# Kernel optimization log

Hardware: AMD Instinct MI355X
Metric: run time of the kernel (lower is better)

Reference implementation:

```python
import jax, jax.numpy as jnp
import numpy as np

B, S, D, H = 2, 2048, 1024, 16
HD = D // H
EPS = 1e-5

def gelu_tanh(x):
    # GPT-2 tanh approximation of GELU
    c = np.sqrt(2.0 / np.pi).astype(np.float32)
    return 0.5 * x * (1.0 + jnp.tanh(c * (x + 0.044715 * x * x * x)))

def layernorm(x, gamma, beta):
    mu = jnp.mean(x, axis=-1, keepdims=True)
    var = jnp.mean(jnp.square(x - mu), axis=-1, keepdims=True)
    return (x - mu) * jax.lax.rsqrt(var + EPS) * gamma + beta

def setup_inputs() -> dict:
    key = jax.random.key(0)
    ks = jax.random.split(key, 16)
    std = 0.02
    def w(k, shape):
        return jax.random.normal(k, shape, dtype=jnp.float32) * std
    return {
        "x": jax.random.normal(ks[0], (B, S, D), dtype=jnp.float32),
        "Wq": w(ks[1], (D, D)), "bq": jnp.zeros((D,), jnp.float32),
        "Wk": w(ks[2], (D, D)), "bk": jnp.zeros((D,), jnp.float32),
        "Wv": w(ks[3], (D, D)), "bv": jnp.zeros((D,), jnp.float32),
        "Wp": w(ks[4], (D, D)), "bp": jnp.zeros((D,), jnp.float32),
        "g0": jnp.ones((D,), jnp.float32), "beta0": jnp.zeros((D,), jnp.float32),
        "W1": w(ks[5], (D, 4 * D)), "b1": jnp.zeros((4 * D,), jnp.float32),
        "W2": w(ks[6], (4 * D, D)), "b2": jnp.zeros((D,), jnp.float32),
        "g1": jnp.ones((D,), jnp.float32), "beta1": jnp.zeros((D,), jnp.float32),
    }

def reference(x, Wq, bq, Wk, bk, Wv, bv, Wp, bp, g0, beta0, W1, b1, W2, b2, g1, beta1):
    b, s, d = x.shape
    # --- causal self-attention (naive full score matrix, as in source) ---
    q = (x @ Wq + bq).reshape(b, s, H, HD).transpose(0, 2, 1, 3)  # [b,h,s,hd]
    k = (x @ Wk + bk).reshape(b, s, H, HD).transpose(0, 2, 1, 3)
    v = (x @ Wv + bv).reshape(b, s, H, HD).transpose(0, 2, 1, 3)
    scores = jnp.einsum('bhqd,bhkd->bhqk', q, k) * (1.0 / np.sqrt(HD))
    mask = jnp.tril(jnp.ones((s, s), dtype=x.dtype))  # lower-triangular causal mask
    scores = scores * mask - 1e10 * (1.0 - mask)
    attn = jax.nn.softmax(scores, axis=-1)
    y = jnp.einsum('bhqk,bhkd->bhqd', attn, v)
    y = y.transpose(0, 2, 1, 3).reshape(b, s, d)
    a = y @ Wp + bp
    # --- post-LN MLP block ---
    x = x + a
    h = layernorm(x, g0, beta0)
    h = gelu_tanh(h @ W1 + b1)
    h = h @ W2 + b2
    x = x + h
    return layernorm(x, g1, beta1)
```

## Files before the change

### kernel.cpp

```cpp
#include <hip/hip_runtime.h>
#include <stdint.h>

#define S_LEN 2048
#define DIM   1024
#define NH    16
#define HDIM  64
#define MTOK  4096
#define DFF   4096

#define QS 0.18033688011112042f

typedef short bf16x8 __attribute__((ext_vector_type(8)));
typedef float f32x4  __attribute__((ext_vector_type(4)));
typedef float f32x16 __attribute__((ext_vector_type(16)));
typedef unsigned int u32x4 __attribute__((ext_vector_type(4)));

__device__ __forceinline__ unsigned short f2bf(float f) {
  unsigned int u = __float_as_uint(f);
  u += 0x7fffu + ((u >> 16) & 1u);
  return (unsigned short)(u >> 16);
}

__device__ __forceinline__ unsigned cvtpk(float a, float b) {
  unsigned r;
  asm("v_cvt_pk_bf16_f32 %0, %1, %2" : "=v"(r) : "v"(a), "v"(b));
  return r;
}

__device__ __forceinline__ float gelu_f(float x) {
  const float c = 0.7978845608028654f;
  float u = c * (x + 0.044715f * x * x * x);
  return 0.5f * x * (1.0f + tanhf(u));
}

__device__ __forceinline__ void gld_lds16(const void* g, void* lds) {
  using gu32p = __attribute__((address_space(1))) unsigned int*;
  using lu32p = __attribute__((address_space(3))) unsigned int*;
  __builtin_amdgcn_global_load_lds((gu32p)g, (lu32p)lds, 16, 0, 0);
}

__global__ __launch_bounds__(256) void cast_f32_bf16(const float* __restrict__ x,
                                                     unsigned short* __restrict__ xb) {
  const size_t i = (size_t)blockIdx.x * 256 + threadIdx.x;
  const float4 a = ((const float4*)x)[2 * i];
  const float4 b = ((const float4*)x)[2 * i + 1];
  ushort4 p0, p1;
  p0.x = f2bf(a.x); p0.y = f2bf(a.y); p0.z = f2bf(a.z); p0.w = f2bf(a.w);
  p1.x = f2bf(b.x); p1.y = f2bf(b.y); p1.z = f2bf(b.z); p1.w = f2bf(b.w);
  ((ushort4*)xb)[2 * i]     = p0;
  ((ushort4*)xb)[2 * i + 1] = p1;
}

__global__ __launch_bounds__(256) void tcast_k(const float* __restrict__ W,
                                               unsigned short* __restrict__ Wt,
                                               int K, int N, float scale) {
  __shared__ float tile[32][33];
  const int tx = threadIdx.x & 31, ty = threadIdx.x >> 5;
  const int n0 = blockIdx.x * 32, k0 = blockIdx.y * 32;
#pragma unroll
  for (int i = 0; i < 4; i++)
    tile[ty + 8 * i][tx] = W[(size_t)(k0 + ty + 8 * i) * N + n0 + tx];
  __syncthreads();
#pragma unroll
  for (int i = 0; i < 4; i++)
    Wt[(size_t)(n0 + ty + 8 * i) * K + k0 + tx] = f2bf(tile[tx][ty + 8 * i] * scale);
}

__global__ __launch_bounds__(256) void bcat_k(const float* __restrict__ bq,
                                              const float* __restrict__ bk,
                                              const float* __restrict__ bv,
                                              float* __restrict__ bqkv) {
  const int t = blockIdx.x * 256 + threadIdx.x;
  float v;
  if (t < 1024)      v = bq[t] * QS;
  else if (t < 2048) v = bk[t - 1024];
  else               v = bv[t - 2048];
  bqkv[t] = v;
}

__global__ __launch_bounds__(256) void vtrans_k(const unsigned short* __restrict__ qkv,
                                                unsigned short* __restrict__ vT) {
  __shared__ unsigned short tile[64][65];
  const int bh = blockIdx.y, b = bh >> 4, h = bh & 15;
  const int s0 = blockIdx.x * 64;
  const int t = threadIdx.x;
#pragma unroll
  for (int i = 0; i < 16; i++) {
    int idx = i * 256 + t, r = idx >> 6, c = idx & 63;
    tile[r][c] = qkv[(size_t)(b * S_LEN + s0 + r) * 3072 + 2048 + h * HDIM + c];
  }
  __syncthreads();
#pragma unroll
  for (int i = 0; i < 16; i++) {
    int idx = i * 256 + t, d = idx >> 6, s = idx & 63;
    vT[(size_t)(bh * HDIM + d) * S_LEN + s0 + s] = tile[s][d];
  }
}

template <int EPI>
__global__ __launch_bounds__(256) void gemm_bt(const unsigned short* __restrict__ A,
                                               const unsigned short* __restrict__ Bt,
                                               const float* __restrict__ bias,
                                               const float* __restrict__ resid,
                                               void* __restrict__ Cout,
                                               int M, int N, int K) {
  __shared__ alignas(16) short As[128 * 32];
  __shared__ alignas(16) short Bs[128 * 32];
  const int t = threadIdx.x;
  const int w = t >> 6, lane = t & 63;
  const int m0 = blockIdx.y * 128, n0 = blockIdx.x * 128;
  const int wr = (w >> 1) * 64, wc = (w & 1) * 64;
  const int lr = lane & 15, lg = lane >> 4;

  f32x4 acc[4][4] = {};

  const int off0 = w * 2048 + lane * 16;
  const int r0 = off0 >> 6, c0 = (off0 & 63) >> 1;
  const int off1 = off0 + 1024;
  const int r1 = off1 >> 6, c1 = (off1 & 63) >> 1;

  const unsigned short* Ag0 = A + (size_t)(m0 + r0) * K + c0;
  const unsigned short* Ag1 = A + (size_t)(m0 + r1) * K + c1;
  const unsigned short* Bg0 = Bt + (size_t)(n0 + r0) * K + c0;
  const unsigned short* Bg1 = Bt + (size_t)(n0 + r1) * K + c1;
  char* AsB = (char*)As;
  char* BsB = (char*)Bs;

  for (int k0 = 0; k0 < K; k0 += 32) {
    gld_lds16(Ag0 + k0, AsB + w * 2048);
    gld_lds16(Ag1 + k0, AsB + w * 2048 + 1024);
    gld_lds16(Bg0 + k0, BsB + w * 2048);
    gld_lds16(Bg1 + k0, BsB + w * 2048 + 1024);
    __syncthreads();
    bf16x8 af[4], bfr[4];
#pragma unroll
    for (int i = 0; i < 4; i++) {
      af[i]  = *reinterpret_cast<const bf16x8*>(As + (wr + i * 16 + lr) * 32 + lg * 8);
      bfr[i] = *reinterpret_cast<const bf16x8*>(Bs + (wc + i * 16 + lr) * 32 + lg * 8);
    }
#pragma unroll
    for (int mi = 0; mi < 4; mi++)
#pragma unroll
      for (int ni = 0; ni < 4; ni++)
        acc[mi][ni] = __builtin_amdgcn_mfma_f32_16x16x32_bf16(af[mi], bfr[ni],
                                                              acc[mi][ni], 0, 0, 0);
    __syncthreads();
  }

  const int colb = n0 + wc + lr;
  const int rowb = m0 + wr + lg * 4;
#pragma unroll
  for (int ni = 0; ni < 4; ni++) {
    const int col = colb + ni * 16;
    const float bv = bias[col];
#pragma unroll
    for (int mi = 0; mi < 4; mi++) {
#pragma unroll
      for (int j = 0; j < 4; j++) {
        const int row = rowb + mi * 16 + j;
        const size_t idx = (size_t)row * N + col;
        float v = acc[mi][ni][j] + bv;
        if constexpr (EPI == 0) {
          ((unsigned short*)Cout)[idx] = f2bf(v);
        } else if constexpr (EPI == 1) {
          ((unsigned short*)Cout)[idx] = f2bf(gelu_f(v));
        } else {
          ((float*)Cout)[idx] = v + resid[idx];
        }
      }
    }
  }
}

__global__ __launch_bounds__(128) void attn32_k(const unsigned short* __restrict__ qkv,
                                                const unsigned short* __restrict__ vT,
                                                unsigned short* __restrict__ y) {
  __shared__ float smem[2][64][33];
  __shared__ float msh[2][64], lsh[2][64];

  const int t = threadIdx.x, w = t >> 6, lane = t & 63;
  const int ql = lane & 31, hi = lane >> 5;
  const int bh = blockIdx.x, bb = bh >> 4, hh = bh & 15;
  const int qt = 63 - blockIdx.y;
  const int half = w;
  const int q0 = qt * 32;

  const unsigned short* qp = qkv + (size_t)(bb * S_LEN + q0 + ql) * 3072 + hh * HDIM + hi * 8;
  const bf16x8 qf0 = *(const bf16x8*)(qp);
  const bf16x8 qf1 = *(const bf16x8*)(qp + 16);
  const bf16x8 qf2 = *(const bf16x8*)(qp + 32);
  const bf16x8 qf3 = *(const bf16x8*)(qp + 48);

  const unsigned short* kbp = qkv + (size_t)(bb * S_LEN) * 3072 + 1024 + hh * HDIM + hi * 8;
  const unsigned short* vbp = vT + (size_t)(bh * HDIM + ql) * (size_t)S_LEN + hi * 8;

  f32x16 acc0 = {}, acc1 = {};
  float m = -1e30f, l = 0.f;

  const int start = half * 32;

  const unsigned short* kp0 = kbp + (size_t)(start + ql) * 3072;
  bf16x8 kc0 = *(const bf16x8*)(kp0);
  bf16x8 kc1 = *(const bf16x8*)(kp0 + 16);
  bf16x8 kc2 = *(const bf16x8*)(kp0 + 32);
  bf16x8 kc3 = *(const bf16x8*)(kp0 + 48);

  for (int t0 = start; t0 <= q0; t0 += 64) {
    const unsigned short* vp = vbp + t0;
    const bf16x8 vf0 = *(const bf16x8*)(vp);
    const bf16x8 vf1 = *(const bf16x8*)(vp + 32 * S_LEN);
    const bf16x8 vf2 = *(const bf16x8*)(vp + 16);
    const bf16x8 vf3 = *(const bf16x8*)(vp + 32 * S_LEN + 16);

    __builtin_amdgcn_s_setprio(1);
    f32x16 st = {};
    st = __builtin_amdgcn_mfma_f32_32x32x16_bf16(kc0, qf0, st, 0, 0, 0);
    st = __builtin_amdgcn_mfma_f32_32x32x16_bf16(kc1, qf1, st, 0, 0, 0);
    st = __builtin_amdgcn_mfma_f32_32x32x16_bf16(kc2, qf2, st, 0, 0, 0);
    st = __builtin_amdgcn_mfma_f32_32x32x16_bf16(kc3, qf3, st, 0, 0, 0);
    __builtin_amdgcn_s_setprio(0);

    const int t1 = (t0 + 64 <= q0) ? (t0 + 64) : t0;
    const unsigned short* kpn = kbp + (size_t)(t1 + ql) * 3072;
    const bf16x8 kn0 = *(const bf16x8*)(kpn);
    const bf16x8 kn1 = *(const bf16x8*)(kpn + 16);
    const bf16x8 kn2 = *(const bf16x8*)(kpn + 32);
    const bf16x8 kn3 = *(const bf16x8*)(kpn + 48);

    if (t0 == q0) {
#pragma unroll
      for (int r = 0; r < 16; r++) {
        const int key = (r & 3) + 8 * (r >> 2) + 4 * hi;
        if (key > ql) st[r] = -1e30f;
      }
    }
    float pm = st[0];
#pragma unroll
    for (int r = 1; r < 16; r++) pm = fmaxf(pm, st[r]);
    pm = fmaxf(pm, __shfl_xor(pm, 32));
    if (!__all(pm - m <= 8.f)) {
      const float mn = fmaxf(m, pm);
      const float rs = exp2f(m - mn);
      l *= rs;
#pragma unroll
      for (int r = 0; r < 16; r++) { acc0[r] *= rs; acc1[r] *= rs; }
      m = mn;
    }
    float sum = 0.f;
#pragma unroll
    for (int r = 0; r < 16; r++) { st[r] = exp2f(st[r] - m); sum += st[r]; }
    sum += __shfl_xor(sum, 32);
    l += sum;

    {
      const unsigned c0 = cvtpk(st[0], st[1]), c1 = cvtpk(st[2], st[3]);
      const unsigned c2 = cvtpk(st[4], st[5]), c3 = cvtpk(st[6], st[7]);
      const unsigned x0 = __shfl_xor(c0, 32), x1 = __shfl_xor(c1, 32);
      const unsigned x2 = __shfl_xor(c2, 32), x3 = __shfl_xor(c3, 32);
      u32x4 fu;
      fu.x = hi ? x2 : c0; fu.y = hi ? x3 : c1;
      fu.z = hi ? c2 : x0; fu.w = hi ? c3 : x1;
      const bf16x8 pf = __builtin_bit_cast(bf16x8, fu);
      __builtin_amdgcn_s_setprio(1);
      acc0 = __builtin_amdgcn_mfma_f32_32x32x16_bf16(vf0, pf, acc0, 0, 0, 0);
      acc1 = __builtin_amdgcn_mfma_f32_32x32x16_bf16(vf1, pf, acc1, 0, 0, 0);
      __builtin_amdgcn_s_setprio(0);
    }
    {
      const unsigned c4 = cvtpk(st[8], st[9]),   c5 = cvtpk(st[10], st[11]);
      const unsigned c6 = cvtpk(st[12], st[13]), c7 = cvtpk(st[14], st[15]);
      const unsigned x4 = __shfl_xor(c4, 32), x5 = __shfl_xor(c5, 32);
      const unsigned x6 = __shfl_xor(c6, 32), x7 = __shfl_xor(c7, 32);
      u32x4 fu;
      fu.x = hi ? x6 : c4; fu.y = hi ? x7 : c5;
      fu.z = hi ? c6 : x4; fu.w = hi ? c7 : x5;
      const bf16x8 pf = __builtin_bit_cast(bf16x8, fu);
      __builtin_amdgcn_s_setprio(1);
      acc0 = __builtin_amdgcn_mfma_f32_32x32x16_bf16(vf2, pf, acc0, 0, 0, 0);
      acc1 = __builtin_amdgcn_mfma_f32_32x32x16_bf16(vf3, pf, acc1, 0, 0, 0);
      __builtin_amdgcn_s_setprio(0);
    }
    kc0 = kn0; kc1 = kn1; kc2 = kn2; kc3 = kn3;
  }

#pragma unroll
  for (int r = 0; r < 16; r++) {
    smem[w][lane][r]      = acc0[r];
    smem[w][lane][16 + r] = acc1[r];
  }
  msh[w][lane] = m; lsh[w][lane] = l;
  __syncthreads();
  if (half) return;

  const int pw = w ^ 1;
  const float mB = msh[pw][lane], lB = lsh[pw][lane];
  const float mm = fmaxf(m, mB);
  float sA = exp2f(m - mm), sB = exp2f(mB - mm);
  const float linv = 1.f / (l * sA + lB * sB);
  sA *= linv; sB *= linv;

  unsigned* tp = (unsigned*)&smem[w][0][0];
  const float* pa = &smem[pw][lane][0];
#pragma unroll
  for (int j = 0; j < 8; j++) {
    const int wd = (j & 1) + 4 * (j >> 1) + 2 * hi;
    const float a0 = acc0[2 * j] * sA + pa[2 * j] * sB;
    const float b0 = acc0[2 * j + 1] * sA + pa[2 * j + 1] * sB;
    tp[ql * 34 + wd] = cvtpk(a0, b0);
    const float a1 = acc1[2 * j] * sA + pa[16 + 2 * j] * sB;
    const float b1 = acc1[2 * j + 1] * sA + pa[16 + 2 * j + 1] * sB;
    tp[ql * 34 + 16 + wd] = cvtpk(a1, b1);
  }
  unsigned* yu = (unsigned*)y;
  const size_t yrow = (size_t)(bb * S_LEN + q0 + ql) * (DIM / 2) + hh * (HDIM / 2) + hi * 16;
#pragma unroll
  for (int i = 0; i < 8; i++) {
    const uint2 d2 = *(const uint2*)&tp[ql * 34 + hi * 16 + 2 * i];
    *(uint2*)&yu[yrow + 2 * i] = d2;
  }
}

template <int OUTBF>
__global__ __launch_bounds__(256) void ln_k(const float* __restrict__ X,
                                            const float* __restrict__ g,
                                            const float* __restrict__ be,
                                            void* __restrict__ out) {
  const int row = blockIdx.x, t = threadIdx.x;
  const float4 v = ((const float4*)(X + (size_t)row * DIM))[t];
  float s  = v.x + v.y + v.z + v.w;
  float s2 = v.x * v.x + v.y * v.y + v.z * v.z + v.w * v.w;
#pragma unroll
  for (int o = 32; o >= 1; o >>= 1) {
    s  += __shfl_down(s, o);
    s2 += __shfl_down(s2, o);
  }
  __shared__ float red[8];
  if ((t & 63) == 0) { red[t >> 6] = s; red[4 + (t >> 6)] = s2; }
  __syncthreads();
  s  = red[0] + red[1] + red[2] + red[3];
  s2 = red[4] + red[5] + red[6] + red[7];
  const float mu  = s * (1.0f / DIM);
  const float var = s2 * (1.0f / DIM) - mu * mu;
  const float r   = rsqrtf(var + 1e-5f);
  const float4 gv = ((const float4*)g)[t];
  const float4 bv = ((const float4*)be)[t];
  const float o0 = (v.x - mu) * r * gv.x + bv.x;
  const float o1 = (v.y - mu) * r * gv.y + bv.y;
  const float o2 = (v.z - mu) * r * gv.z + bv.z;
  const float o3 = (v.w - mu) * r * gv.w + bv.w;
  if constexpr (OUTBF) {
    ushort4 p; p.x = f2bf(o0); p.y = f2bf(o1); p.z = f2bf(o2); p.w = f2bf(o3);
    ((ushort4*)out)[(size_t)row * 256 + t] = p;
  } else {
    float4 p; p.x = o0; p.y = o1; p.z = o2; p.w = o3;
    ((float4*)out)[(size_t)row * 256 + t] = p;
  }
}

extern "C" void kernel_launch(void* const* d_in, const int* in_sizes, int n_in,
                              void* d_out, int out_size, void* d_ws, size_t ws_size,
                              hipStream_t stream) {
  const float* x   = (const float*)d_in[0];
  const float* Wq  = (const float*)d_in[1];
  const float* bq  = (const float*)d_in[2];
  const float* Wk  = (const float*)d_in[3];
  const float* bk  = (const float*)d_in[4];
  const float* Wv  = (const float*)d_in[5];
  const float* bv  = (const float*)d_in[6];
  const float* Wp  = (const float*)d_in[7];
  const float* bp  = (const float*)d_in[8];
  const float* g0  = (const float*)d_in[9];
  const float* be0 = (const float*)d_in[10];
  const float* W1  = (const float*)d_in[11];
  const float* b1  = (const float*)d_in[12];
  const float* W2  = (const float*)d_in[13];
  const float* b2  = (const float*)d_in[14];
  const float* g1  = (const float*)d_in[15];
  const float* be1 = (const float*)d_in[16];

  char* ws = (char*)d_ws;
  const size_t MB = 1ull << 20;
  unsigned short* xb    = (unsigned short*)(ws + 0 * MB);
  unsigned short* qkvb  = (unsigned short*)(ws + 8 * MB);
  unsigned short* vTb   = (unsigned short*)(ws + 32 * MB);
  unsigned short* yb    = (unsigned short*)(ws + 40 * MB);
  float*          bqkv  = (float*)(ws + 48 * MB);
  float*          x1    = (float*)(ws + 48 * MB);
  unsigned short* hb    = (unsigned short*)(ws + 64 * MB);
  unsigned short* WqkvT = (unsigned short*)(ws + 72 * MB);
  unsigned short* WpT   = (unsigned short*)(ws + 78 * MB);
  unsigned short* W1T   = (unsigned short*)(ws + 80 * MB);
  unsigned short* W2T   = (unsigned short*)(ws + 88 * MB);
  unsigned short* h1    = (unsigned short*)(ws + 8 * MB);
  float*          x2    = (float*)(ws + 64 * MB);

  cast_f32_bf16<<<2048, 256, 0, stream>>>(x, xb);
  tcast_k<<<dim3(32, 32), 256, 0, stream>>>(Wq, WqkvT,               1024, 1024, QS);
  tcast_k<<<dim3(32, 32), 256, 0, stream>>>(Wk, WqkvT + 1024 * 1024, 1024, 1024, 1.f);
  tcast_k<<<dim3(32, 32), 256, 0, stream>>>(Wv, WqkvT + 2048 * 1024, 1024, 1024, 1.f);
  tcast_k<<<dim3(32, 32), 256, 0, stream>>>(Wp, WpT, 1024, 1024, 1.f);
  tcast_k<<<dim3(128, 32), 256, 0, stream>>>(W1, W1T, 1024, 4096, 1.f);
  tcast_k<<<dim3(32, 128), 256, 0, stream>>>(W2, W2T, 4096, 1024, 1.f);
  bcat_k<<<12, 256, 0, stream>>>(bq, bk, bv, bqkv);

  gemm_bt<0><<<dim3(24, 32), 256, 0, stream>>>(xb, WqkvT, bqkv, nullptr, qkvb, MTOK, 3072, 1024);

  vtrans_k<<<dim3(32, 32), 256, 0, stream>>>(qkvb, vTb);
  attn32_k<<<dim3(32, 64), 128, 0, stream>>>(qkvb, vTb, yb);

  gemm_bt<2><<<dim3(8, 32), 256, 0, stream>>>(yb, WpT, bp, x, x1, MTOK, DIM, DIM);
  ln_k<1><<<4096, 256, 0, stream>>>(x1, g0, be0, hb);

  gemm_bt<1><<<dim3(32, 32), 256, 0, stream>>>(hb, W1T, b1, nullptr, h1, MTOK, DFF, DIM);
  gemm_bt<2><<<dim3(8, 32), 256, 0, stream>>>(h1, W2T, b2, x1, x2, MTOK, DIM, DFF);
  ln_k<0><<<4096, 256, 0, stream>>>(x2, g1, be1, d_out);
}
```

Measured before the change: 471.8 us.

## Double-buffer GEMM LDS tiles with K=64 steps and block swizzle

```diff
diff --git a/kernel.cpp b/kernel.cpp
--- a/kernel.cpp
+++ b/kernel.cpp
@@ -98,53 +98,71 @@
 }
 
 template <int EPI>
-__global__ __launch_bounds__(256) void gemm_bt(const unsigned short* __restrict__ A,
-                                               const unsigned short* __restrict__ Bt,
-                                               const float* __restrict__ bias,
-                                               const float* __restrict__ resid,
-                                               void* __restrict__ Cout,
-                                               int M, int N, int K) {
-  __shared__ alignas(16) short As[128 * 32];
-  __shared__ alignas(16) short Bs[128 * 32];
-  const int t = threadIdx.x;
-  const int w = t >> 6, lane = t & 63;
-  const int m0 = blockIdx.y * 128, n0 = blockIdx.x * 128;
+__global__ __launch_bounds__(256, 2) void gemm2p(const unsigned short* __restrict__ A,
+                                                 const unsigned short* __restrict__ Bt,
+                                                 const float* __restrict__ bias,
+                                                 const float* __restrict__ resid,
+                                                 void* __restrict__ Cout,
+                                                 int M, int N, int K) {
+  __shared__ alignas(16) short As[2][128 * 64];
+  __shared__ alignas(16) short Bs[2][128 * 64];
+  const int t = threadIdx.x, w = t >> 6, lane = t & 63;
+
+  const int gx = gridDim.x, nwg = gx * gridDim.y;
+  const int bid = blockIdx.x + gx * blockIdx.y;
+  const int swz = (bid & 7) * (nwg >> 3) + (bid >> 3);
+  const int m0 = (swz / gx) * 128, n0 = (swz % gx) * 128;
+
   const int wr = (w >> 1) * 64, wc = (w & 1) * 64;
   const int lr = lane & 15, lg = lane >> 4;
 
   f32x4 acc[4][4] = {};
 
-  const int off0 = w * 2048 + lane * 16;
-  const int r0 = off0 >> 6, c0 = (off0 & 63) >> 1;
-  const int off1 = off0 + 1024;
-  const int r1 = off1 >> 6, c1 = (off1 & 63) >> 1;
-
-  const unsigned short* Ag0 = A + (size_t)(m0 + r0) * K + c0;
-  const unsigned short* Ag1 = A + (size_t)(m0 + r1) * K + c1;
-  const unsigned short* Bg0 = Bt + (size_t)(n0 + r0) * K + c0;
-  const unsigned short* Bg1 = Bt + (size_t)(n0 + r1) * K + c1;
-  char* AsB = (char*)As;
-  char* BsB = (char*)Bs;
-
-  for (int k0 = 0; k0 < K; k0 += 32) {
-    gld_lds16(Ag0 + k0, AsB + w * 2048);
-    gld_lds16(Ag1 + k0, AsB + w * 2048 + 1024);
-    gld_lds16(Bg0 + k0, BsB + w * 2048);
-    gld_lds16(Bg1 + k0, BsB + w * 2048 + 1024);
+  const int sr = w * 32 + (lane >> 3);
+  const int sc = (lane & 7) * 8;
+  const unsigned short* Ag = A + (size_t)(m0 + sr) * K + sc;
+  const unsigned short* Bg = Bt + (size_t)(n0 + sr) * K + sc;
+  const int dbase = w * 4096 + lane * 16;
+
+  const int NT = K >> 6;
+
+#pragma unroll
+  for (int i = 0; i < 4; i++) {
+    gld_lds16(Ag + (size_t)(i * 8) * K, (char*)As[0] + dbase + i * 1024);
+    gld_lds16(Bg + (size_t)(i * 8) * K, (char*)Bs[0] + dbase + i * 1024);
+  }
+  __syncthreads();
+
+  int cur = 0;
+  for (int kt = 0; kt < NT; ++kt) {
+    if (kt + 1 < NT) {
+      const int k1 = (kt + 1) << 6;
+#pragma unroll
+      for (int i = 0; i < 4; i++) {
+        gld_lds16(Ag + (size_t)(i * 8) * K + k1, (char*)As[cur ^ 1] + dbase + i * 1024);
+        gld_lds16(Bg + (size_t)(i * 8) * K + k1, (char*)Bs[cur ^ 1] + dbase + i * 1024);
+      }
+    }
+    bf16x8 af[2][4], bfr[2][4];
+#pragma unroll
+    for (int ks = 0; ks < 2; ks++)
+#pragma unroll
+      for (int i = 0; i < 4; i++) {
+        af[ks][i]  = *reinterpret_cast<const bf16x8*>(&As[cur][(wr + i * 16 + lr) * 64 + ks * 32 + lg * 8]);
+        bfr[ks][i] = *reinterpret_cast<const bf16x8*>(&Bs[cur][(wc + i * 16 + lr) * 64 + ks * 32 + lg * 8]);
+      }
+    __builtin_amdgcn_s_setprio(1);
+#pragma unroll
+    for (int ks = 0; ks < 2; ks++)
+#pragma unroll
+      for (int mi = 0; mi < 4; mi++)
+#pragma unroll
+        for (int ni = 0; ni < 4; ni++)
+          acc[mi][ni] = __builtin_amdgcn_mfma_f32_16x16x32_bf16(af[ks][mi], bfr[ks][ni],
+                                                                acc[mi][ni], 0, 0, 0);
+    __builtin_amdgcn_s_setprio(0);
     __syncthreads();
-    bf16x8 af[4], bfr[4];
-#pragma unroll
-    for (int i = 0; i < 4; i++) {
-      af[i]  = *reinterpret_cast<const bf16x8*>(As + (wr + i * 16 + lr) * 32 + lg * 8);
-      bfr[i] = *reinterpret_cast<const bf16x8*>(Bs + (wc + i * 16 + lr) * 32 + lg * 8);
-    }
-#pragma unroll
-    for (int mi = 0; mi < 4; mi++)
-#pragma unroll
-      for (int ni = 0; ni < 4; ni++)
-        acc[mi][ni] = __builtin_amdgcn_mfma_f32_16x16x32_bf16(af[mi], bfr[ni],
-                                                              acc[mi][ni], 0, 0, 0);
-    __syncthreads();
+    cur ^= 1;
   }
 
   const int colb = n0 + wc + lr;
@@ -403,15 +421,15 @@
   tcast_k<<<dim3(32, 128), 256, 0, stream>>>(W2, W2T, 4096, 1024, 1.f);
   bcat_k<<<12, 256, 0, stream>>>(bq, bk, bv, bqkv);
 
-  gemm_bt<0><<<dim3(24, 32), 256, 0, stream>>>(xb, WqkvT, bqkv, nullptr, qkvb, MTOK, 3072, 1024);
+  gemm2p<0><<<dim3(24, 32), 256, 0, stream>>>(xb, WqkvT, bqkv, nullptr, qkvb, MTOK, 3072, 1024);
 
   vtrans_k<<<dim3(32, 32), 256, 0, stream>>>(qkvb, vTb);
   attn32_k<<<dim3(32, 64), 128, 0, stream>>>(qkvb, vTb, yb);
 
-  gemm_bt<2><<<dim3(8, 32), 256, 0, stream>>>(yb, WpT, bp, x, x1, MTOK, DIM, DIM);
+  gemm2p<2><<<dim3(8, 32), 256, 0, stream>>>(yb, WpT, bp, x, x1, MTOK, DIM, DIM);
   ln_k<1><<<4096, 256, 0, stream>>>(x1, g0, be0, hb);
 
-  gemm_bt<1><<<dim3(32, 32), 256, 0, stream>>>(hb, W1T, b1, nullptr, h1, MTOK, DFF, DIM);
-  gemm_bt<2><<<dim3(8, 32), 256, 0, stream>>>(h1, W2T, b2, x1, x2, MTOK, DIM, DFF);
+  gemm2p<1><<<dim3(32, 32), 256, 0, stream>>>(hb, W1T, b1, nullptr, h1, MTOK, DFF, DIM);
+  gemm2p<2><<<dim3(8, 32), 256, 0, stream>>>(h1, W2T, b2, x1, x2, MTOK, DIM, DFF);
   ln_k<0><<<4096, 256, 0, stream>>>(x2, g1, be1, d_out);
 }
```

Result: faster. 462.1 us (-2.0%).
